# Kernel tuning notes

Hardware: AMD Instinct MI355X
Metric: run time of the kernel (lower is better)

The kernel has to match this reference:

```python
import jax, jax.numpy as jnp
import numpy as np

NUM_HEADS = 32
HEAD_SIZE = 128
NUM_KV_HEADS = 8
BLOCK_SIZE = 16
X = 8  # vector width of key cache last dim
NUM_SEQS = 64
MAX_BLOCKS = 64  # blocks per sequence
NUM_BLOCKS = NUM_SEQS * MAX_BLOCKS  # 4096
MAX_CONTEXT = MAX_BLOCKS * BLOCK_SIZE  # 1024
SCALE = 0.08838834764831845  # 1/sqrt(128)


def setup_inputs() -> dict:
    key = jax.random.key(0)
    ks = jax.random.split(key, 6)
    query = jax.random.normal(ks[0], (NUM_SEQS, NUM_HEADS * HEAD_SIZE), jnp.float32)
    k_new = jax.random.normal(ks[1], (NUM_SEQS, NUM_KV_HEADS * HEAD_SIZE), jnp.float32)
    v_new = jax.random.normal(ks[2], (NUM_SEQS, NUM_KV_HEADS * HEAD_SIZE), jnp.float32)
    key_cache = jax.random.normal(ks[3], (NUM_BLOCKS, NUM_KV_HEADS, HEAD_SIZE // X, BLOCK_SIZE, X), jnp.float32)
    value_cache = jax.random.normal(ks[4], (NUM_BLOCKS, NUM_KV_HEADS, HEAD_SIZE, BLOCK_SIZE), jnp.float32)
    # every sequence owns MAX_BLOCKS distinct physical blocks
    block_tables = jnp.arange(NUM_SEQS * MAX_BLOCKS, dtype=jnp.int32).reshape(NUM_SEQS, MAX_BLOCKS)
    context_lens = jax.random.randint(ks[5], (NUM_SEQS,), 1, MAX_CONTEXT + 1, jnp.int32)
    # slot of the current token (position context_len-1), as produced by the scheduler
    last = context_lens - 1
    slot_mapping = (block_tables[jnp.arange(NUM_SEQS), last // BLOCK_SIZE] * BLOCK_SIZE
                    + last % BLOCK_SIZE).astype(jnp.int32)
    return dict(query=query, key=k_new, value=v_new, key_cache=key_cache,
                value_cache=value_cache, block_tables=block_tables,
                context_lens=context_lens, slot_mapping=slot_mapping)


def _paged_attention(query, key, value, key_cache, value_cache,
                     block_tables, context_lens, slot_mapping):
    S = query.shape[0]
    G = NUM_HEADS // NUM_KV_HEADS  # queries per kv head (head_mapping)
    q = query.reshape(S, NUM_KV_HEADS, G, HEAD_SIZE)
    k_new = key.reshape(S, NUM_KV_HEADS, HEAD_SIZE // X, X)
    v_new = value.reshape(S, NUM_KV_HEADS, HEAD_SIZE)
    # reshape_and_cache: scatter the new token's K/V into the paged caches
    blk = slot_mapping // BLOCK_SIZE
    off = slot_mapping % BLOCK_SIZE
    kc = key_cache.at[blk, :, :, off, :].set(k_new)   # [T,KV,HS/X,X] -> cache
    vc = value_cache.at[blk, :, :, off].set(v_new)    # [T,KV,HS]    -> cache
    # gather paged KV: [S, MB, KV, HS/X, BS, X] -> [S, MAX_CONTEXT, KV, HS]
    keys = kc[block_tables].transpose(0, 1, 4, 2, 3, 5).reshape(S, MAX_CONTEXT, NUM_KV_HEADS, HEAD_SIZE)
    # [S, MB, KV, HS, BS] -> [S, MAX_CONTEXT, KV, HS]
    vals = vc[block_tables].transpose(0, 1, 4, 2, 3).reshape(S, MAX_CONTEXT, NUM_KV_HEADS, HEAD_SIZE)
    scores = jnp.einsum('sngd,stnd->sngt', q, keys) * SCALE  # [S,KV,G,T]
    valid = jnp.arange(MAX_CONTEXT)[None, :] < context_lens[:, None]
    scores = jnp.where(valid[:, None, None, :], scores, jnp.finfo(scores.dtype).min)
    probs = jax.nn.softmax(scores, axis=-1)
    out = jnp.einsum('sngt,stnd->sngd', probs, vals)
    return out.reshape(S, NUM_HEADS * HEAD_SIZE)


def reference(query, key, value, key_cache, value_cache, block_tables, context_lens, slot_mapping):
    return _paged_attention(query, key, value, key_cache, value_cache,
                            block_tables, context_lens, slot_mapping)
```

## Files before the change

kernel.cpp:

```cpp
#include <hip/hip_runtime.h>
#include <math.h>

#define NUM_HEADS    32
#define HEAD_SIZE    128
#define NUM_KV       8
#define GQ           4
#define BLOCK_SZ     16
#define NUM_SEQS     64
#define MAX_BLOCKS   64
#define MAX_CONTEXT  1024
#define SPLIT        128
#define NSPLIT       8
#define NPAIR        (NUM_SEQS * NUM_KV)
#define SCALEF       0.08838834764831845f
#define LOG2E        1.4426950408889634f
#define SC2          (SCALEF * LOG2E)


__global__ __launch_bounds__(64, 3) void pa_main(
    const float* __restrict__ q,
    const float* __restrict__ knew,
    const float* __restrict__ vnew,
    const float* __restrict__ kcache,
    const float* __restrict__ vcache,
    const int* __restrict__ btab,
    const int* __restrict__ ctx,
    float* __restrict__ o_ws,
    float* __restrict__ l_ws)
{
    const int split = blockIdx.x >> 9;
    const int pair  = blockIdx.x & 511;
    const int s = pair >> 3;
    const int h = pair & 7;
    const int L = ctx[s];
    const int start = split * SPLIT;
    if (start >= L) return;
    const int end  = min(start + SPLIT, L);
    const int nblk = (end - start + 15) >> 4;
    const int lunit = pair * NSPLIT + split;

    const int lane    = threadIdx.x;
    const int p_q     = lane >> 2;
    const int quarter = lane & 3;

    const int lastpos  = L - 1;
    const int b_last   = (lastpos >> 4) - (start >> 4);
    const int off_last = lastpos & 15;
    const bool hasfix  = (b_last >= 0) && (b_last < nblk);

    __shared__ float4 q_lds4[128];
    __shared__ float4 e_lds4[16];

    {
        const float4* qb = (const float4*)(q + s * 4096 + h * 512);
        q_lds4[lane]      = qb[lane];
        q_lds4[lane + 64] = qb[lane + 64];
    }

    float lsum[GQ], o[GQ][8];
#pragma unroll
    for (int g = 0; g < GQ; g++) {
        lsum[g] = 0.f;
#pragma unroll
        for (int j = 0; j < 8; j++) o[g][j] = 0.f;
    }

    const int koff = (quarter >> 1) * 128 + p_q * 8 + (quarter & 1) * 4;
    const float* knb = knew + s * 1024 + h * 128 + (quarter >> 1) * 8 + (quarter & 1) * 4;
    const float* vnb = vnew + s * 1024 + h * 128;

    const int pidx = s * MAX_BLOCKS + (start >> 4);

    for (int b = 0; b < nblk; b++) {
        const int phys = btab[pidx + b];
        const float* kb = kcache + (size_t)phys * 16384 + h * 2048;
        const float* vb = vcache + (size_t)phys * 16384 + h * 2048;
        const bool fix = hasfix && (b == b_last);

        float4 kr[8];
#pragma unroll
        for (int it = 0; it < 8; it++)
            kr[it] = *(const float4*)(kb + it * 256 + koff);
        float4 vr[8];
#pragma unroll
        for (int j = 0; j < 8; j++)
            vr[j] = *(const float4*)(vb + j * 256 + lane * 4);

        if (fix && p_q == off_last) {
#pragma unroll
            for (int it = 0; it < 8; it++)
                kr[it] = *(const float4*)(knb + it * 16);
        }

        float part[GQ] = {0.f, 0.f, 0.f, 0.f};
#pragma unroll
        for (int it = 0; it < 8; it++) {
#pragma unroll
            for (int g = 0; g < GQ; g++) {
                float4 q4 = q_lds4[g * 32 + it * 4 + quarter];
                part[g] += kr[it].x * q4.x + kr[it].y * q4.y
                         + kr[it].z * q4.z + kr[it].w * q4.w;
            }
        }

#pragma unroll
        for (int g = 0; g < GQ; g++) {
            part[g] += __shfl_xor(part[g], 1);
            part[g] += __shfl_xor(part[g], 2);
        }

        const int  pos   = start + b * 16 + p_q;
        const bool valid = pos <= lastpos;

        float e[GQ];
#pragma unroll
        for (int g = 0; g < GQ; g++) {
            float ex = __builtin_amdgcn_exp2f(part[g] * SC2);
            e[g] = valid ? ex : 0.f;
            lsum[g] += e[g];
        }

        if (quarter == 0) e_lds4[p_q] = make_float4(e[0], e[1], e[2], e[3]);
        const float4 ev0 = e_lds4[(quarter << 2) + 0];
        const float4 ev1 = e_lds4[(quarter << 2) + 1];
        const float4 ev2 = e_lds4[(quarter << 2) + 2];
        const float4 ev3 = e_lds4[(quarter << 2) + 3];

        if (fix) {
            const bool mine = (quarter == (off_last >> 2));
            const int c = off_last & 3;
#pragma unroll
            for (int j = 0; j < 8; j++) {
                const float vn = vnb[j * 16 + p_q];
                if (c == 0)      { if (mine) vr[j].x = vn; }
                else if (c == 1) { if (mine) vr[j].y = vn; }
                else if (c == 2) { if (mine) vr[j].z = vn; }
                else             { if (mine) vr[j].w = vn; }
            }
        }

#pragma unroll
        for (int j = 0; j < 8; j++) {
            o[0][j] += ev0.x * vr[j].x + ev1.x * vr[j].y + ev2.x * vr[j].z + ev3.x * vr[j].w;
            o[1][j] += ev0.y * vr[j].x + ev1.y * vr[j].y + ev2.y * vr[j].z + ev3.y * vr[j].w;
            o[2][j] += ev0.z * vr[j].x + ev1.z * vr[j].y + ev2.z * vr[j].z + ev3.z * vr[j].w;
            o[3][j] += ev0.w * vr[j].x + ev1.w * vr[j].y + ev2.w * vr[j].z + ev3.w * vr[j].w;
        }
    }

#pragma unroll
    for (int g = 0; g < GQ; g++)
#pragma unroll
        for (int j = 0; j < 8; j++) {
            o[g][j] += __shfl_xor(o[g][j], 1);
            o[g][j] += __shfl_xor(o[g][j], 2);
        }
#pragma unroll
    for (int g = 0; g < GQ; g++) {
        lsum[g] += __shfl_xor(lsum[g], 4);
        lsum[g] += __shfl_xor(lsum[g], 8);
        lsum[g] += __shfl_xor(lsum[g], 16);
        lsum[g] += __shfl_xor(lsum[g], 32);
    }

    float* ob = o_ws + (size_t)lunit * 512;
#pragma unroll
    for (int j = 0; j < 8; j++) {
        float val = (quarter == 0) ? o[0][j]
                  : (quarter == 1) ? o[1][j]
                  : (quarter == 2) ? o[2][j] : o[3][j];
        ob[j * 64 + lane] = val;
    }
    if (lane == 0) {
        float* lw = l_ws + lunit * 4;
        lw[0] = lsum[0]; lw[1] = lsum[1]; lw[2] = lsum[2]; lw[3] = lsum[3];
    }
}

__global__ __launch_bounds__(256) void pa_combine(
    const float* __restrict__ o_ws, const float* __restrict__ l_ws,
    const int* __restrict__ ctx, float* __restrict__ out)
{
    const int pair = blockIdx.x;
    const int s = pair >> 3, h = pair & 7;
    const int L = ctx[s];
    const int nsp = (L + SPLIT - 1) >> 7;
    const int t = threadIdx.x;
    __shared__ float lds[512];

#pragma unroll
    for (int r = 0; r < 2; r++) {
        const int f = t + r * 256;
        const int g = f & 3;
        float acc = 0.f, lacc = 0.f;
        for (int sp = 0; sp < nsp; sp++) {
            lacc += l_ws[(pair * 8 + sp) * 4 + g];
            acc  += o_ws[(size_t)(pair * 8 + sp) * 512 + f];
        }
        lds[f] = acc / lacc;
    }
    __syncthreads();
#pragma unroll
    for (int r = 0; r < 2; r++) {
        const int of = t + r * 256;
        const int g = of >> 7, d = of & 127;
        out[s * 4096 + h * 512 + of] = lds[d * 4 + g];
    }
}

extern "C" void kernel_launch(void* const* d_in, const int* in_sizes, int n_in,
                              void* d_out, int out_size, void* d_ws, size_t ws_size,
                              hipStream_t stream) {
    const float* query = (const float*)d_in[0];
    const float* knew  = (const float*)d_in[1];
    const float* vnew  = (const float*)d_in[2];
    const float* kcache = (const float*)d_in[3];
    const float* vcache = (const float*)d_in[4];
    const int* btab    = (const int*)d_in[5];
    const int* ctx     = (const int*)d_in[6];
    float* out  = (float*)d_out;
    float* o_ws = (float*)d_ws;
    float* l_ws = o_ws + 4096 * 512;

    pa_main<<<dim3(4096), dim3(64), 0, stream>>>(query, knew, vnew, kcache, vcache,
                                                 btab, ctx, o_ws, l_ws);
    pa_combine<<<dim3(512), dim3(256), 0, stream>>>(o_ws, l_ws, ctx, out);
}
```

Baseline: 586.5 us.

## Split each split's KV blocks across two wavefronts with LDS reduction

The main kernel now launches 128 threads per workgroup. Two wavefronts take alternating 16-token KV blocks within the same 128-token split, and their partial outputs and sums are combined through shared memory before one wave writes the result. The goal is more memory requests in flight and shorter serial loops for this latency-bound kernel. The cost is an extra barrier, some LDS traffic, and a looser launch-bounds hint that may change register allocation and occupancy.

```diff
diff --git a/kernel.cpp b/kernel.cpp
--- a/kernel.cpp
+++ b/kernel.cpp
@@ -17,7 +17,7 @@
 #define SC2          (SCALEF * LOG2E)
 
 
-__global__ __launch_bounds__(64, 3) void pa_main(
+__global__ __launch_bounds__(128) void pa_main(
     const float* __restrict__ q,
     const float* __restrict__ knew,
     const float* __restrict__ vnew,
@@ -39,7 +39,8 @@
     const int nblk = (end - start + 15) >> 4;
     const int lunit = pair * NSPLIT + split;
 
-    const int lane    = threadIdx.x;
+    const int w       = threadIdx.x >> 6;
+    const int lane    = threadIdx.x & 63;
     const int p_q     = lane >> 2;
     const int quarter = lane & 3;
 
@@ -49,7 +50,9 @@
     const bool hasfix  = (b_last >= 0) && (b_last < nblk);
 
     __shared__ float4 q_lds4[128];
-    __shared__ float4 e_lds4[16];
+    __shared__ float4 e_lds4[2][16];
+    __shared__ float  o_red[512];
+    __shared__ float  l_red[4];
 
     {
         const float4* qb = (const float4*)(q + s * 4096 + h * 512);
@@ -71,7 +74,7 @@
 
     const int pidx = s * MAX_BLOCKS + (start >> 4);
 
-    for (int b = 0; b < nblk; b++) {
+    for (int b = w; b < nblk; b += 2) {
         const int phys = btab[pidx + b];
         const float* kb = kcache + (size_t)phys * 16384 + h * 2048;
         const float* vb = vcache + (size_t)phys * 16384 + h * 2048;
@@ -120,11 +123,11 @@
             lsum[g] += e[g];
         }
 
-        if (quarter == 0) e_lds4[p_q] = make_float4(e[0], e[1], e[2], e[3]);
-        const float4 ev0 = e_lds4[(quarter << 2) + 0];
-        const float4 ev1 = e_lds4[(quarter << 2) + 1];
-        const float4 ev2 = e_lds4[(quarter << 2) + 2];
-        const float4 ev3 = e_lds4[(quarter << 2) + 3];
+        if (quarter == 0) e_lds4[w][p_q] = make_float4(e[0], e[1], e[2], e[3]);
+        const float4 ev0 = e_lds4[w][(quarter << 2) + 0];
+        const float4 ev1 = e_lds4[w][(quarter << 2) + 1];
+        const float4 ev2 = e_lds4[w][(quarter << 2) + 2];
+        const float4 ev3 = e_lds4[w][(quarter << 2) + 3];
 
         if (fix) {
             const bool mine = (quarter == (off_last >> 2));
@@ -163,17 +166,32 @@
         lsum[g] += __shfl_xor(lsum[g], 32);
     }
 
-    float* ob = o_ws + (size_t)lunit * 512;
-#pragma unroll
-    for (int j = 0; j < 8; j++) {
-        float val = (quarter == 0) ? o[0][j]
-                  : (quarter == 1) ? o[1][j]
-                  : (quarter == 2) ? o[2][j] : o[3][j];
-        ob[j * 64 + lane] = val;
-    }
-    if (lane == 0) {
-        float* lw = l_ws + lunit * 4;
-        lw[0] = lsum[0]; lw[1] = lsum[1]; lw[2] = lsum[2]; lw[3] = lsum[3];
+    float val[8];
+#pragma unroll
+    for (int j = 0; j < 8; j++)
+        val[j] = (quarter == 0) ? o[0][j]
+               : (quarter == 1) ? o[1][j]
+               : (quarter == 2) ? o[2][j] : o[3][j];
+
+    if (w == 1) {
+#pragma unroll
+        for (int j = 0; j < 8; j++) o_red[j * 64 + lane] = val[j];
+        if (lane == 0) {
+            l_red[0] = lsum[0]; l_red[1] = lsum[1];
+            l_red[2] = lsum[2]; l_red[3] = lsum[3];
+        }
+    }
+    __syncthreads();
+    if (w == 0) {
+        float* ob = o_ws + (size_t)lunit * 512;
+#pragma unroll
+        for (int j = 0; j < 8; j++)
+            ob[j * 64 + lane] = val[j] + o_red[j * 64 + lane];
+        if (lane == 0) {
+            float* lw = l_ws + lunit * 4;
+            lw[0] = lsum[0] + l_red[0]; lw[1] = lsum[1] + l_red[1];
+            lw[2] = lsum[2] + l_red[2]; lw[3] = lsum[3] + l_red[3];
+        }
     }
 }
 
@@ -222,7 +240,7 @@
     float* o_ws = (float*)d_ws;
     float* l_ws = o_ws + 4096 * 512;
 
-    pa_main<<<dim3(4096), dim3(64), 0, stream>>>(query, knew, vnew, kcache, vcache,
-                                                 btab, ctx, o_ws, l_ws);
+    pa_main<<<dim3(4096), dim3(128), 0, stream>>>(query, knew, vnew, kcache, vcache,
+                                                  btab, ctx, o_ws, l_ws);
     pa_combine<<<dim3(512), dim3(256), 0, stream>>>(o_ws, l_ws, ctx, out);
 }
```

After: 491.0 us. 1.19x faster.

## Merge the eight KV heads of a sequence split into one 512-thread workgroup

Applied to the files above, without the earlier changes.

The main kernel now launches one 512-thread workgroup per (split, sequence), with each wave handling one KV head, in place of one 64-thread workgroup per (split, head pair). A workgroup barrier at the top of each block iteration keeps the waves in lockstep, so the eight heads fetch the same physical block at roughly the same time and reuse the block-table read and cache locality. The cost is an extra barrier per block, coarser scheduling with fewer and larger workgroups, and a looser launch bound that may change register allocation.

```diff
diff --git a/kernel.cpp b/kernel.cpp
--- a/kernel.cpp
+++ b/kernel.cpp
@@ -17,7 +17,7 @@
 #define SC2          (SCALEF * LOG2E)
 
 
-__global__ __launch_bounds__(64, 3) void pa_main(
+__global__ __launch_bounds__(512) void pa_main(
     const float* __restrict__ q,
     const float* __restrict__ knew,
     const float* __restrict__ vnew,
@@ -28,33 +28,32 @@
     float* __restrict__ o_ws,
     float* __restrict__ l_ws)
 {
-    const int split = blockIdx.x >> 9;
-    const int pair  = blockIdx.x & 511;
-    const int s = pair >> 3;
-    const int h = pair & 7;
+    const int split = blockIdx.x >> 6;
+    const int s     = blockIdx.x & 63;
     const int L = ctx[s];
     const int start = split * SPLIT;
     if (start >= L) return;
     const int end  = min(start + SPLIT, L);
     const int nblk = (end - start + 15) >> 4;
-    const int lunit = pair * NSPLIT + split;
-
-    const int lane    = threadIdx.x;
+
+    const int h       = threadIdx.x >> 6;
+    const int lane    = threadIdx.x & 63;
     const int p_q     = lane >> 2;
     const int quarter = lane & 3;
+    const int lunit   = (s * NUM_KV + h) * NSPLIT + split;
 
     const int lastpos  = L - 1;
     const int b_last   = (lastpos >> 4) - (start >> 4);
     const int off_last = lastpos & 15;
     const bool hasfix  = (b_last >= 0) && (b_last < nblk);
 
-    __shared__ float4 q_lds4[128];
-    __shared__ float4 e_lds4[16];
+    __shared__ float4 q_lds4[8][128];
+    __shared__ float4 e_lds4[8][16];
 
     {
         const float4* qb = (const float4*)(q + s * 4096 + h * 512);
-        q_lds4[lane]      = qb[lane];
-        q_lds4[lane + 64] = qb[lane + 64];
+        q_lds4[h][lane]      = qb[lane];
+        q_lds4[h][lane + 64] = qb[lane + 64];
     }
 
     float lsum[GQ], o[GQ][8];
@@ -72,6 +71,8 @@
     const int pidx = s * MAX_BLOCKS + (start >> 4);
 
     for (int b = 0; b < nblk; b++) {
+        __builtin_amdgcn_s_barrier();
+
         const int phys = btab[pidx + b];
         const float* kb = kcache + (size_t)phys * 16384 + h * 2048;
         const float* vb = vcache + (size_t)phys * 16384 + h * 2048;
@@ -97,7 +98,7 @@
         for (int it = 0; it < 8; it++) {
 #pragma unroll
             for (int g = 0; g < GQ; g++) {
-                float4 q4 = q_lds4[g * 32 + it * 4 + quarter];
+                float4 q4 = q_lds4[h][g * 32 + it * 4 + quarter];
                 part[g] += kr[it].x * q4.x + kr[it].y * q4.y
                          + kr[it].z * q4.z + kr[it].w * q4.w;
             }
@@ -120,11 +121,11 @@
             lsum[g] += e[g];
         }
 
-        if (quarter == 0) e_lds4[p_q] = make_float4(e[0], e[1], e[2], e[3]);
-        const float4 ev0 = e_lds4[(quarter << 2) + 0];
-        const float4 ev1 = e_lds4[(quarter << 2) + 1];
-        const float4 ev2 = e_lds4[(quarter << 2) + 2];
-        const float4 ev3 = e_lds4[(quarter << 2) + 3];
+        if (quarter == 0) e_lds4[h][p_q] = make_float4(e[0], e[1], e[2], e[3]);
+        const float4 ev0 = e_lds4[h][(quarter << 2) + 0];
+        const float4 ev1 = e_lds4[h][(quarter << 2) + 1];
+        const float4 ev2 = e_lds4[h][(quarter << 2) + 2];
+        const float4 ev3 = e_lds4[h][(quarter << 2) + 3];
 
         if (fix) {
             const bool mine = (quarter == (off_last >> 2));
@@ -222,7 +223,7 @@
     float* o_ws = (float*)d_ws;
     float* l_ws = o_ws + 4096 * 512;
 
-    pa_main<<<dim3(4096), dim3(64), 0, stream>>>(query, knew, vnew, kcache, vcache,
+    pa_main<<<dim3(512), dim3(512), 0, stream>>>(query, knew, vnew, kcache, vcache,
                                                  btab, ctx, o_ws, l_ws);
     pa_combine<<<dim3(512), dim3(256), 0, stream>>>(o_ws, l_ws, ctx, out);
 }
```

New measurement: 510.7 us. -12.9%, faster.
